# Optimization experiments

Hardware: AMD Instinct MI355X
Metric: run time of the kernel (lower is better)

The kernel has to match this reference:

```python
import jax, jax.numpy as jnp
import numpy as np

N_HEADS = 8
OUT_DIM = 64
LEAKY_SLOPE = 0.2


def setup_inputs() -> dict:
    key = jax.random.key(0)
    k1, k2, k3 = jax.random.split(key, 3)
    N, IN_DIM = 4096, 256
    x = jax.random.normal(k1, (N, IN_DIM), dtype=jnp.float32)
    # nn.Linear(in_dim, out_dim*n_heads, bias=False): weight shape (out*heads, in)
    W = jax.random.normal(k2, (OUT_DIM * N_HEADS, IN_DIM), dtype=jnp.float32) * (1.0 / np.sqrt(IN_DIM))
    # attention vector, xavier-ish scale
    attn = jax.random.normal(k3, (1, N_HEADS, 2 * OUT_DIM), dtype=jnp.float32) * 0.1
    return {"x": x, "W": W, "attn": attn}


def reference(x, W, attn):
    N = x.shape[0]
    # Wx: (N, H, D)
    Wx = (x @ W.T).reshape(N, N_HEADS, OUT_DIM)
    # The torch code concats src/tgt then dots with attn; this decomposes exactly:
    # e[i,j,h] = leaky_relu( Wx[i,h]·a_src[h] + Wx[j,h]·a_tgt[h] )
    a_src = attn[0, :, :OUT_DIM]   # (H, D)
    a_tgt = attn[0, :, OUT_DIM:]   # (H, D)
    s = jnp.einsum('nhd,hd->nh', Wx, a_src)  # (N, H) score of row index (src)
    t = jnp.einsum('nhd,hd->nh', Wx, a_tgt)  # (N, H) score of col index (tgt)
    e = jax.nn.leaky_relu(s[:, None, :] + t[None, :, :], LEAKY_SLOPE)  # (N, N, H)
    a = jax.nn.softmax(e, axis=1)  # softmax over dim=1 (neighbors j)
    # out[i,h,d] = sum_j a[i,j,h] * Wx[j,h,d]
    out = jnp.einsum('ijh,jhd->ihd', a, Wx)
    return out.reshape(N, N_HEADS * OUT_DIM)  # concat=True
```

## Files before the change

kernel.cpp:

```cpp
#include <hip/hip_runtime.h>
#include <hip/hip_bf16.h>

#define NN 4096
#define KD 256
#define NH 8
#define DD 64
#define HD 512
#define SLOPE 0.2f

__global__ __launch_bounds__(256) void gemm_st(const float* __restrict__ x,
                                               const float* __restrict__ W,
                                               const float* __restrict__ attn,
                                               float* __restrict__ Wx,
                                               float* __restrict__ sH,
                                               float* __restrict__ tH) {
    const int b = blockIdx.x;
    const int bmTile = (b & 7) * 8 + ((b >> 3) & 7);
    const int h = b >> 6;
    const int bn = h * 64;
    const int bm = bmTile * 64;
    __shared__ float As[32][68];
    __shared__ float Bs[32][68];
    const int tid = threadIdx.x;
    const int tx = tid & 15, ty = tid >> 4;
    const int srow = tid >> 2;
    const int skq  = (tid & 3) * 8;
    float acc[4][4] = {};
    for (int k0 = 0; k0 < KD; k0 += 32) {
        float4 a0 = *(const float4*)&x[(bm + srow) * KD + k0 + skq];
        float4 a1 = *(const float4*)&x[(bm + srow) * KD + k0 + skq + 4];
        float4 b0 = *(const float4*)&W[(bn + srow) * KD + k0 + skq];
        float4 b1 = *(const float4*)&W[(bn + srow) * KD + k0 + skq + 4];
        __syncthreads();
        As[skq + 0][srow] = a0.x; As[skq + 1][srow] = a0.y;
        As[skq + 2][srow] = a0.z; As[skq + 3][srow] = a0.w;
        As[skq + 4][srow] = a1.x; As[skq + 5][srow] = a1.y;
        As[skq + 6][srow] = a1.z; As[skq + 7][srow] = a1.w;
        Bs[skq + 0][srow] = b0.x; Bs[skq + 1][srow] = b0.y;
        Bs[skq + 2][srow] = b0.z; Bs[skq + 3][srow] = b0.w;
        Bs[skq + 4][srow] = b1.x; Bs[skq + 5][srow] = b1.y;
        Bs[skq + 6][srow] = b1.z; Bs[skq + 7][srow] = b1.w;
        __syncthreads();
#pragma unroll
        for (int kk = 0; kk < 32; ++kk) {
            float4 a = *(const float4*)&As[kk][ty * 4];
            float4 bb = *(const float4*)&Bs[kk][tx * 4];
            acc[0][0] += a.x * bb.x; acc[0][1] += a.x * bb.y; acc[0][2] += a.x * bb.z; acc[0][3] += a.x * bb.w;
            acc[1][0] += a.y * bb.x; acc[1][1] += a.y * bb.y; acc[1][2] += a.y * bb.z; acc[1][3] += a.y * bb.w;
            acc[2][0] += a.z * bb.x; acc[2][1] += a.z * bb.y; acc[2][2] += a.z * bb.z; acc[2][3] += a.z * bb.w;
            acc[3][0] += a.w * bb.x; acc[3][1] += a.w * bb.y; acc[3][2] += a.w * bb.z; acc[3][3] += a.w * bb.w;
        }
    }
#pragma unroll
    for (int m = 0; m < 4; ++m)
        *(float4*)&Wx[(bm + ty * 4 + m) * HD + bn + tx * 4] = *(const float4*)&acc[m][0];
    float4 as4 = *(const float4*)&attn[h * 128 + tx * 4];
    float4 at4 = *(const float4*)&attn[h * 128 + 64 + tx * 4];
#pragma unroll
    for (int m = 0; m < 4; ++m) {
        float s = acc[m][0] * as4.x + acc[m][1] * as4.y + acc[m][2] * as4.z + acc[m][3] * as4.w;
        float t = acc[m][0] * at4.x + acc[m][1] * at4.y + acc[m][2] * at4.z + acc[m][3] * at4.w;
#pragma unroll
        for (int off = 1; off < 16; off <<= 1) {
            s += __shfl_xor(s, off, 16);
            t += __shfl_xor(t, off, 16);
        }
        if (tx == 0) {
            sH[h * NN + bm + ty * 4 + m] = s;
            tH[h * NN + bm + ty * 4 + m] = t;
        }
    }
}

__global__ __launch_bounds__(512) void count_scatter(const float* __restrict__ tH,
                                                     const float* __restrict__ sH,
                                                     int* __restrict__ sortedIdx,
                                                     float* __restrict__ expT,
                                                     float* __restrict__ expT2,
                                                     int* __restrict__ cIdx) {
    const int h  = blockIdx.y;
    const int jg = blockIdx.x;
    const int tid = threadIdx.x;
    const int w  = tid >> 6;
    const int jj = tid & 63;
    const int j  = jg * 64 + jj;
    const int qj = jg >> 3;
    __shared__ float tl[NN];
    __shared__ int rsum[8][64], csum[8][64];
    {
        const float4* src4 = (const float4*)&tH[h * NN];
        float4* dst4 = (float4*)tl;
        for (int p4 = tid; p4 < NN / 4; p4 += 512) dst4[p4] = src4[p4];
    }
    __syncthreads();
    const float myT  = tl[j];
    const float negS = -sH[h * NN + j];
    const float4* t4 = (const float4*)&tl[w * 512];
    int rx = 0, ry = 0, rz = 0, rw = 0;
    int cx = 0, cy = 0, cz = 0, cw = 0;
    if (w < qj) {
#pragma unroll 8
        for (int p4 = 0; p4 < 128; ++p4) {
            float4 v = t4[p4];
            rx += (v.x <= myT); ry += (v.y <= myT); rz += (v.z <= myT); rw += (v.w <= myT);
            cx += (v.x <= negS); cy += (v.y <= negS); cz += (v.z <= negS); cw += (v.w <= negS);
        }
    } else if (w > qj) {
#pragma unroll 8
        for (int p4 = 0; p4 < 128; ++p4) {
            float4 v = t4[p4];
            rx += (v.x < myT); ry += (v.y < myT); rz += (v.z < myT); rw += (v.w < myT);
            cx += (v.x <= negS); cy += (v.y <= negS); cz += (v.z <= negS); cw += (v.w <= negS);
        }
    } else {
        const int pbase = w * 512;
#pragma unroll 4
        for (int p4 = 0; p4 < 128; ++p4) {
            float4 v = t4[p4];
            int p = pbase + p4 * 4;
            rx += (v.x < myT) | ((v.x == myT) & ((p + 0) < j));
            ry += (v.y < myT) | ((v.y == myT) & ((p + 1) < j));
            rz += (v.z < myT) | ((v.z == myT) & ((p + 2) < j));
            rw += (v.w < myT) | ((v.w == myT) & ((p + 3) < j));
            cx += (v.x <= negS); cy += (v.y <= negS); cz += (v.z <= negS); cw += (v.w <= negS);
        }
    }
    rsum[w][jj] = (rx + ry) + (rz + rw);
    csum[w][jj] = (cx + cy) + (cz + cw);
    __syncthreads();
    if (tid < 64) {
        const int jt = jg * 64 + tid;
        int R  = ((rsum[0][tid] + rsum[1][tid]) + (rsum[2][tid] + rsum[3][tid]))
               + ((rsum[4][tid] + rsum[5][tid]) + (rsum[6][tid] + rsum[7][tid]));
        int CS = ((csum[0][tid] + csum[1][tid]) + (csum[2][tid] + csum[3][tid]))
               + ((csum[4][tid] + csum[5][tid]) + (csum[6][tid] + csum[7][tid]));
        const float tv = tl[jt];
        sortedIdx[h * NN + R] = jt;
        expT [h * NN + R] = expf(tv);
        expT2[h * NN + R] = expf(SLOPE * tv);
        cIdx[h * NN + jt] = CS;
    }
}

__global__ __launch_bounds__(256) void local_prefix(const float* __restrict__ Wx,
                                                    const int* __restrict__ sortedIdx,
                                                    const float* __restrict__ expT,
                                                    const float* __restrict__ expT2,
                                                    float* __restrict__ localW,
                                                    float* __restrict__ localW2,
                                                    float* __restrict__ chunkTotW,
                                                    float* __restrict__ chunkTotW2,
                                                    float* __restrict__ localZ,
                                                    float* __restrict__ localZ2,
                                                    float* __restrict__ chunkZtot,
                                                    float* __restrict__ chunkZtot2) {
    const int c = blockIdx.x, h = blockIdx.y;
    const int tid = threadIdx.x;
    const int wid = tid >> 6, d = tid & 63;
    const int base = h * NN + c * 64;
    __shared__ float sums[4][64], sums2[4][64];
    float run = 0.f, run2 = 0.f;
    float ex[16], ex2[16];
#pragma unroll
    for (int kk = 0; kk < 16; ++kk) {
        int k = wid * 16 + kk;
        int j = sortedIdx[base + k];
        float w  = expT[base + k];
        float w2 = expT2[base + k];
        float v = Wx[j * HD + h * DD + d];
        ex[kk]  = run;  run  += w  * v;
        ex2[kk] = run2; run2 += w2 * v;
    }
    sums[wid][d] = run; sums2[wid][d] = run2;
    __syncthreads();
    float off = 0.f, off2 = 0.f;
    for (int w = 0; w < 4; ++w)
        if (w < wid) { off += sums[w][d]; off2 += sums2[w][d]; }
#pragma unroll
    for (int kk = 0; kk < 16; ++kk) {
        int k = wid * 16 + kk;
        localW [(h * NN + c * 64 + k) * 64 + d] = ex[kk]  + off;
        localW2[(h * NN + c * 64 + k) * 64 + d] = ex2[kk] + off2;
    }
    if (wid == 3) {
        chunkTotW [(h * 64 + c) * 64 + d] = off  + run;
        chunkTotW2[(h * 64 + c) * 64 + d] = off2 + run2;
    }
    if (wid == 0) {
        float z0 = expT[base + d];
        float z = z0;
#pragma unroll
        for (int o = 1; o < 64; o <<= 1) { float n = __shfl_up(z, o, 64); if (d >= o) z += n; }
        localZ[h * NN + c * 64 + d] = z - z0;
        if (d == 63) chunkZtot[h * 64 + c] = z;
    } else if (wid == 1) {
        float z0 = expT2[base + d];
        float z = z0;
#pragma unroll
        for (int o = 1; o < 64; o <<= 1) { float n = __shfl_up(z, o, 64); if (d >= o) z += n; }
        localZ2[h * NN + c * 64 + d] = z - z0;
        if (d == 63) chunkZtot2[h * 64 + c] = z;
    }
}

__global__ __launch_bounds__(256) void chunk_scan(float* __restrict__ chunkTotW,
                                                  float* __restrict__ chunkTotW2,
                                                  float* __restrict__ chunkZtot,
                                                  float* __restrict__ chunkZtot2,
                                                  float* __restrict__ totW,
                                                  float* __restrict__ totW2,
                                                  float* __restrict__ Ztot,
                                                  float* __restrict__ Ztot2) {
    const int h = blockIdx.x;
    const int tid = threadIdx.x;
    const int lane = tid & 63;
    __shared__ float cw[64 * 64];
    __shared__ float cw2[64 * 64];
    __shared__ float zb[64], zb2[64];
#pragma unroll
    for (int it = 0; it < 16; ++it) {
        int lin = it * 256 + tid;
        cw[lin]  = chunkTotW [h * 4096 + lin];
        cw2[lin] = chunkTotW2[h * 4096 + lin];
    }
    if (tid >= 128 && tid < 192) zb[lane]  = chunkZtot [h * 64 + lane];
    if (tid >= 192)              zb2[lane] = chunkZtot2[h * 64 + lane];
    __syncthreads();
    if (tid < 64) {
        float acc = 0.f;
        for (int c = 0; c < 64; ++c) { int idx = c * 64 + tid; float t = cw[idx]; cw[idx] = acc; acc += t; }
        totW[h * 64 + tid] = acc;
    } else if (tid < 128) {
        int d = tid - 64;
        float acc = 0.f;
        for (int c = 0; c < 64; ++c) { int idx = c * 64 + d; float t = cw2[idx]; cw2[idx] = acc; acc += t; }
        totW2[h * 64 + d] = acc;
    } else if (tid < 192) {
        float z0 = zb[lane];
        float z = z0;
#pragma unroll
        for (int o = 1; o < 64; o <<= 1) { float n = __shfl_up(z, o, 64); if (lane >= o) z += n; }
        chunkZtot[h * 64 + lane] = z - z0;
        if (lane == 63) Ztot[h] = z;
    } else {
        float z0 = zb2[lane];
        float z = z0;
#pragma unroll
        for (int o = 1; o < 64; o <<= 1) { float n = __shfl_up(z, o, 64); if (lane >= o) z += n; }
        chunkZtot2[h * 64 + lane] = z - z0;
        if (lane == 63) Ztot2[h] = z;
    }
    __syncthreads();
#pragma unroll
    for (int it = 0; it < 16; ++it) {
        int lin = it * 256 + tid;
        chunkTotW [h * 4096 + lin] = cw[lin];
        chunkTotW2[h * 4096 + lin] = cw2[lin];
    }
}

__global__ __launch_bounds__(256) void out_kernel(const float* __restrict__ sH,
                                                  const int* __restrict__ cIdx,
                                                  const float* __restrict__ localW,
                                                  const float* __restrict__ localW2,
                                                  const float* __restrict__ chunkTotW,
                                                  const float* __restrict__ chunkTotW2,
                                                  const float* __restrict__ localZ,
                                                  const float* __restrict__ localZ2,
                                                  const float* __restrict__ chunkZtot,
                                                  const float* __restrict__ chunkZtot2,
                                                  const float* __restrict__ totW,
                                                  const float* __restrict__ totW2,
                                                  const float* __restrict__ Ztot,
                                                  const float* __restrict__ Ztot2,
                                                  float* __restrict__ out) {
    const int h = blockIdx.y;
    const int i = blockIdx.x * 4 + (threadIdx.x >> 6);
    const int d = threadIdx.x & 63;
    const float sv = sH[h * NN + i];
    const int c = cIdx[h * NN + i];
    const float es  = expf(sv);
    const float es2 = expf(SLOPE * sv);
    float wpos, wneg, zp, zn;
    if (c == NN) {
        wpos = 0.f; zp = 0.f;
        wneg = totW2[h * 64 + d];
        zn   = Ztot2[h];
    } else {
        float pw  = localW [(h * NN + c) * 64 + d] + chunkTotW [(h * 64 + (c >> 6)) * 64 + d];
        float pw2 = localW2[(h * NN + c) * 64 + d] + chunkTotW2[(h * 64 + (c >> 6)) * 64 + d];
        wpos = totW[h * 64 + d] - pw;
        wneg = pw2;
        float pz  = localZ [h * NN + c] + chunkZtot [h * 64 + (c >> 6)];
        float pz2 = localZ2[h * NN + c] + chunkZtot2[h * 64 + (c >> 6)];
        zp = Ztot[h] - pz;
        zn = pz2;
    }
    out[i * HD + h * DD + d] = (es * wpos + es2 * wneg) / (es * zp + es2 * zn);
}

extern "C" void kernel_launch(void* const* d_in, const int* in_sizes, int n_in,
                              void* d_out, int out_size, void* d_ws, size_t ws_size,
                              hipStream_t stream) {
    const float* x    = (const float*)d_in[0];
    const float* W    = (const float*)d_in[1];
    const float* attn = (const float*)d_in[2];
    float* out = (float*)d_out;

    float* ws = (float*)d_ws;
    size_t o = 0;
    float* Wx        = ws + o; o += (size_t)NN * HD;
    float* sH        = ws + o; o += (size_t)NH * NN;
    float* tH        = ws + o; o += (size_t)NH * NN;
    float* expT      = ws + o; o += (size_t)NH * NN;
    float* expT2     = ws + o; o += (size_t)NH * NN;
    int*   sortedIdx = (int*)(ws + o); o += (size_t)NH * NN;
    int*   cIdx      = (int*)(ws + o); o += (size_t)NH * NN;
    float* localZ    = ws + o; o += (size_t)NH * NN;
    float* localZ2   = ws + o; o += (size_t)NH * NN;
    float* chunkTotW  = ws + o; o += (size_t)NH * 64 * 64;
    float* chunkTotW2 = ws + o; o += (size_t)NH * 64 * 64;
    float* chunkZtot  = ws + o; o += (size_t)NH * 64;
    float* chunkZtot2 = ws + o; o += (size_t)NH * 64;
    float* totW   = ws + o; o += (size_t)NH * 64;
    float* totW2  = ws + o; o += (size_t)NH * 64;
    float* Ztot   = ws + o; o += 64;
    float* Ztot2  = ws + o; o += 64;
    float* localW  = ws + o; o += (size_t)NH * NN * 64;
    float* localW2 = ws + o; o += (size_t)NH * NN * 64;

    gemm_st<<<dim3(512), dim3(256), 0, stream>>>(x, W, attn, Wx, sH, tH);
    count_scatter<<<dim3(64, NH), dim3(512), 0, stream>>>(tH, sH, sortedIdx, expT, expT2, cIdx);
    local_prefix<<<dim3(64, NH), dim3(256), 0, stream>>>(Wx, sortedIdx, expT, expT2, localW, localW2,
                                                         chunkTotW, chunkTotW2, localZ, localZ2, chunkZtot, chunkZtot2);
    chunk_scan<<<dim3(NH), dim3(256), 0, stream>>>(chunkTotW, chunkTotW2, chunkZtot, chunkZtot2,
                                                   totW, totW2, Ztot, Ztot2);
    out_kernel<<<dim3(NN / 4, NH), dim3(256), 0, stream>>>(sH, cIdx, localW, localW2, chunkTotW, chunkTotW2,
                                                           localZ, localZ2, chunkZtot, chunkZtot2,
                                                           totW, totW2, Ztot, Ztot2, out);
}
```

Baseline: 69.51 us.

## Fuse chunk scan into output kernel, binary-search cut index, prefetch GEMM tiles

The chunk_scan kernel is folded into out_kernel. Each block now recomputes the per-head chunk prefix sums in shared memory and finds each row's cut index with a binary search over the sorted t values. Previously count_scatter produced that index with a brute-force count, which is now removed. The GEMM also register-prefetches the next K tile while computing on the current one. The changes save one launch and the O(N^2) comparison work, at the cost of redundant per-block chunk scans and fewer, larger out_kernel blocks (64x8), which may lower parallelism.

```diff
diff --git a/kernel.cpp b/kernel.cpp
--- a/kernel.cpp
+++ b/kernel.cpp
@@ -26,11 +26,11 @@
     const int srow = tid >> 2;
     const int skq  = (tid & 3) * 8;
     float acc[4][4] = {};
+    float4 a0 = *(const float4*)&x[(bm + srow) * KD + skq];
+    float4 a1 = *(const float4*)&x[(bm + srow) * KD + skq + 4];
+    float4 b0 = *(const float4*)&W[(bn + srow) * KD + skq];
+    float4 b1 = *(const float4*)&W[(bn + srow) * KD + skq + 4];
     for (int k0 = 0; k0 < KD; k0 += 32) {
-        float4 a0 = *(const float4*)&x[(bm + srow) * KD + k0 + skq];
-        float4 a1 = *(const float4*)&x[(bm + srow) * KD + k0 + skq + 4];
-        float4 b0 = *(const float4*)&W[(bn + srow) * KD + k0 + skq];
-        float4 b1 = *(const float4*)&W[(bn + srow) * KD + k0 + skq + 4];
         __syncthreads();
         As[skq + 0][srow] = a0.x; As[skq + 1][srow] = a0.y;
         As[skq + 2][srow] = a0.z; As[skq + 3][srow] = a0.w;
@@ -41,6 +41,12 @@
         Bs[skq + 4][srow] = b1.x; Bs[skq + 5][srow] = b1.y;
         Bs[skq + 6][srow] = b1.z; Bs[skq + 7][srow] = b1.w;
         __syncthreads();
+        if (k0 + 32 < KD) {
+            a0 = *(const float4*)&x[(bm + srow) * KD + k0 + 32 + skq];
+            a1 = *(const float4*)&x[(bm + srow) * KD + k0 + 32 + skq + 4];
+            b0 = *(const float4*)&W[(bn + srow) * KD + k0 + 32 + skq];
+            b1 = *(const float4*)&W[(bn + srow) * KD + k0 + 32 + skq + 4];
+        }
 #pragma unroll
         for (int kk = 0; kk < 32; ++kk) {
             float4 a = *(const float4*)&As[kk][ty * 4];
@@ -73,11 +79,10 @@
 }
 
 __global__ __launch_bounds__(512) void count_scatter(const float* __restrict__ tH,
-                                                     const float* __restrict__ sH,
+                                                     float* __restrict__ tsorted,
                                                      int* __restrict__ sortedIdx,
                                                      float* __restrict__ expT,
-                                                     float* __restrict__ expT2,
-                                                     int* __restrict__ cIdx) {
+                                                     float* __restrict__ expT2) {
     const int h  = blockIdx.y;
     const int jg = blockIdx.x;
     const int tid = threadIdx.x;
@@ -86,31 +91,27 @@
     const int j  = jg * 64 + jj;
     const int qj = jg >> 3;
     __shared__ float tl[NN];
-    __shared__ int rsum[8][64], csum[8][64];
+    __shared__ int rsum[8][64];
     {
         const float4* src4 = (const float4*)&tH[h * NN];
         float4* dst4 = (float4*)tl;
         for (int p4 = tid; p4 < NN / 4; p4 += 512) dst4[p4] = src4[p4];
     }
     __syncthreads();
-    const float myT  = tl[j];
-    const float negS = -sH[h * NN + j];
+    const float myT = tl[j];
     const float4* t4 = (const float4*)&tl[w * 512];
     int rx = 0, ry = 0, rz = 0, rw = 0;
-    int cx = 0, cy = 0, cz = 0, cw = 0;
     if (w < qj) {
 #pragma unroll 8
         for (int p4 = 0; p4 < 128; ++p4) {
             float4 v = t4[p4];
             rx += (v.x <= myT); ry += (v.y <= myT); rz += (v.z <= myT); rw += (v.w <= myT);
-            cx += (v.x <= negS); cy += (v.y <= negS); cz += (v.z <= negS); cw += (v.w <= negS);
         }
     } else if (w > qj) {
 #pragma unroll 8
         for (int p4 = 0; p4 < 128; ++p4) {
             float4 v = t4[p4];
             rx += (v.x < myT); ry += (v.y < myT); rz += (v.z < myT); rw += (v.w < myT);
-            cx += (v.x <= negS); cy += (v.y <= negS); cz += (v.z <= negS); cw += (v.w <= negS);
         }
     } else {
         const int pbase = w * 512;
@@ -122,23 +123,19 @@
             ry += (v.y < myT) | ((v.y == myT) & ((p + 1) < j));
             rz += (v.z < myT) | ((v.z == myT) & ((p + 2) < j));
             rw += (v.w < myT) | ((v.w == myT) & ((p + 3) < j));
-            cx += (v.x <= negS); cy += (v.y <= negS); cz += (v.z <= negS); cw += (v.w <= negS);
         }
     }
     rsum[w][jj] = (rx + ry) + (rz + rw);
-    csum[w][jj] = (cx + cy) + (cz + cw);
     __syncthreads();
     if (tid < 64) {
         const int jt = jg * 64 + tid;
         int R  = ((rsum[0][tid] + rsum[1][tid]) + (rsum[2][tid] + rsum[3][tid]))
                + ((rsum[4][tid] + rsum[5][tid]) + (rsum[6][tid] + rsum[7][tid]));
-        int CS = ((csum[0][tid] + csum[1][tid]) + (csum[2][tid] + csum[3][tid]))
-               + ((csum[4][tid] + csum[5][tid]) + (csum[6][tid] + csum[7][tid]));
         const float tv = tl[jt];
+        tsorted[h * NN + R]   = tv;
         sortedIdx[h * NN + R] = jt;
         expT [h * NN + R] = expf(tv);
         expT2[h * NN + R] = expf(SLOPE * tv);
-        cIdx[h * NN + jt] = CS;
     }
 }
 
@@ -203,100 +200,106 @@
     }
 }
 
-__global__ __launch_bounds__(256) void chunk_scan(float* __restrict__ chunkTotW,
-                                                  float* __restrict__ chunkTotW2,
-                                                  float* __restrict__ chunkZtot,
-                                                  float* __restrict__ chunkZtot2,
-                                                  float* __restrict__ totW,
-                                                  float* __restrict__ totW2,
-                                                  float* __restrict__ Ztot,
-                                                  float* __restrict__ Ztot2) {
-    const int h = blockIdx.x;
+__global__ __launch_bounds__(256) void out_kernel(const float* __restrict__ sH,
+                                                  const float* __restrict__ tsorted,
+                                                  const float* __restrict__ localW,
+                                                  const float* __restrict__ localW2,
+                                                  const float* __restrict__ localZ,
+                                                  const float* __restrict__ localZ2,
+                                                  const float* __restrict__ chunkTotW,
+                                                  const float* __restrict__ chunkTotW2,
+                                                  const float* __restrict__ chunkZtot,
+                                                  const float* __restrict__ chunkZtot2,
+                                                  float* __restrict__ out) {
+    const int h  = blockIdx.y;
+    const int ig = blockIdx.x;
     const int tid = threadIdx.x;
-    const int lane = tid & 63;
-    __shared__ float cw[64 * 64];
-    __shared__ float cw2[64 * 64];
-    __shared__ float zb[64], zb2[64];
-#pragma unroll
-    for (int it = 0; it < 16; ++it) {
-        int lin = it * 256 + tid;
-        cw[lin]  = chunkTotW [h * 4096 + lin];
-        cw2[lin] = chunkTotW2[h * 4096 + lin];
-    }
-    if (tid >= 128 && tid < 192) zb[lane]  = chunkZtot [h * 64 + lane];
-    if (tid >= 192)              zb2[lane] = chunkZtot2[h * 64 + lane];
+    __shared__ float ts[NN];
+    __shared__ float scW[65][64];
+    __shared__ float scW2[65][64];
+    __shared__ float scZ[65], scZ2[65];
+    {
+        const float4* src = (const float4*)&tsorted[h * NN];
+        float4* dst = (float4*)ts;
+        for (int p = tid; p < NN / 4; p += 256) dst[p] = src[p];
+        const float4* cw  = (const float4*)&chunkTotW [h * 4096];
+        const float4* cw2 = (const float4*)&chunkTotW2[h * 4096];
+        for (int p = tid; p < 1024; p += 256) {
+            int c = p >> 4, q = p & 15;
+            ((float4*)&scW[c][0])[q]  = cw[p];
+            ((float4*)&scW2[c][0])[q] = cw2[p];
+        }
+        if (tid < 64)                    scZ [tid]      = chunkZtot [h * 64 + tid];
+        else if (tid < 128)              scZ2[tid - 64] = chunkZtot2[h * 64 + tid - 64];
+    }
     __syncthreads();
     if (tid < 64) {
         float acc = 0.f;
-        for (int c = 0; c < 64; ++c) { int idx = c * 64 + tid; float t = cw[idx]; cw[idx] = acc; acc += t; }
-        totW[h * 64 + tid] = acc;
+        for (int c = 0; c < 64; ++c) { float t = scW[c][tid]; scW[c][tid] = acc; acc += t; }
+        scW[64][tid] = acc;
     } else if (tid < 128) {
-        int d = tid - 64;
-        float acc = 0.f;
-        for (int c = 0; c < 64; ++c) { int idx = c * 64 + d; float t = cw2[idx]; cw2[idx] = acc; acc += t; }
-        totW2[h * 64 + d] = acc;
+        int d = tid - 64; float acc = 0.f;
+        for (int c = 0; c < 64; ++c) { float t = scW2[c][d]; scW2[c][d] = acc; acc += t; }
+        scW2[64][d] = acc;
     } else if (tid < 192) {
-        float z0 = zb[lane];
-        float z = z0;
+        int lane = tid & 63;
+        float z0 = scZ[lane]; float z = z0;
 #pragma unroll
         for (int o = 1; o < 64; o <<= 1) { float n = __shfl_up(z, o, 64); if (lane >= o) z += n; }
-        chunkZtot[h * 64 + lane] = z - z0;
-        if (lane == 63) Ztot[h] = z;
+        scZ[lane] = z - z0;
+        if (lane == 63) scZ[64] = z;
     } else {
-        float z0 = zb2[lane];
-        float z = z0;
+        int lane = tid & 63;
+        float z0 = scZ2[lane]; float z = z0;
 #pragma unroll
         for (int o = 1; o < 64; o <<= 1) { float n = __shfl_up(z, o, 64); if (lane >= o) z += n; }
-        chunkZtot2[h * 64 + lane] = z - z0;
-        if (lane == 63) Ztot2[h] = z;
-    }
-    __syncthreads();
-#pragma unroll
-    for (int it = 0; it < 16; ++it) {
-        int lin = it * 256 + tid;
-        chunkTotW [h * 4096 + lin] = cw[lin];
-        chunkTotW2[h * 4096 + lin] = cw2[lin];
-    }
-}
-
-__global__ __launch_bounds__(256) void out_kernel(const float* __restrict__ sH,
-                                                  const int* __restrict__ cIdx,
-                                                  const float* __restrict__ localW,
-                                                  const float* __restrict__ localW2,
-                                                  const float* __restrict__ chunkTotW,
-                                                  const float* __restrict__ chunkTotW2,
-                                                  const float* __restrict__ localZ,
-                                                  const float* __restrict__ localZ2,
-                                                  const float* __restrict__ chunkZtot,
-                                                  const float* __restrict__ chunkZtot2,
-                                                  const float* __restrict__ totW,
-                                                  const float* __restrict__ totW2,
-                                                  const float* __restrict__ Ztot,
-                                                  const float* __restrict__ Ztot2,
-                                                  float* __restrict__ out) {
-    const int h = blockIdx.y;
-    const int i = blockIdx.x * 4 + (threadIdx.x >> 6);
-    const int d = threadIdx.x & 63;
-    const float sv = sH[h * NN + i];
-    const int c = cIdx[h * NN + i];
-    const float es  = expf(sv);
-    const float es2 = expf(SLOPE * sv);
-    float wpos, wneg, zp, zn;
-    if (c == NN) {
-        wpos = 0.f; zp = 0.f;
-        wneg = totW2[h * 64 + d];
-        zn   = Ztot2[h];
-    } else {
-        float pw  = localW [(h * NN + c) * 64 + d] + chunkTotW [(h * 64 + (c >> 6)) * 64 + d];
-        float pw2 = localW2[(h * NN + c) * 64 + d] + chunkTotW2[(h * 64 + (c >> 6)) * 64 + d];
-        wpos = totW[h * 64 + d] - pw;
-        wneg = pw2;
-        float pz  = localZ [h * NN + c] + chunkZtot [h * 64 + (c >> 6)];
-        float pz2 = localZ2[h * NN + c] + chunkZtot2[h * 64 + (c >> 6)];
-        zp = Ztot[h] - pz;
-        zn = pz2;
-    }
-    out[i * HD + h * DD + d] = (es * wpos + es2 * wneg) / (es * zp + es2 * zn);
+        scZ2[lane] = z - z0;
+        if (lane == 63) scZ2[64] = z;
+    }
+    __syncthreads();
+    int   cc[16];
+    float svv[16];
+#pragma unroll
+    for (int p = 0; p < 16; ++p) {
+        const int i = ig * 64 + p * 4 + (tid >> 6);
+        const float sv = sH[h * NN + i];
+        svv[p] = sv;
+        const float negS = -sv;
+        int lo = 0, hi = NN;
+#pragma unroll
+        for (int st = 0; st < 12; ++st) {
+            int mid = (lo + hi) >> 1;
+            bool le = ts[mid] <= negS;
+            lo = le ? mid + 1 : lo;
+            hi = le ? hi : mid;
+        }
+        cc[p] = lo;
+    }
+#pragma unroll
+    for (int p = 0; p < 16; ++p) {
+        const int i = ig * 64 + p * 4 + (tid >> 6);
+        const int d = tid & 63;
+        const int c = cc[p];
+        const float sv = svv[p];
+        const float es  = expf(sv);
+        const float es2 = expf(SLOPE * sv);
+        float wpos, wneg, zp, zn;
+        if (c == NN) {
+            wpos = 0.f; zp = 0.f;
+            wneg = scW2[64][d];
+            zn   = scZ2[64];
+        } else {
+            float pw  = localW [(h * NN + c) * 64 + d] + scW [c >> 6][d];
+            float pw2 = localW2[(h * NN + c) * 64 + d] + scW2[c >> 6][d];
+            wpos = scW[64][d] - pw;
+            wneg = pw2;
+            float pz  = localZ [h * NN + c] + scZ [c >> 6];
+            float pz2 = localZ2[h * NN + c] + scZ2[c >> 6];
+            zp = scZ[64] - pz;
+            zn = pz2;
+        }
+        out[i * HD + h * DD + d] = (es * wpos + es2 * wneg) / (es * zp + es2 * zn);
+    }
 }
 
 extern "C" void kernel_launch(void* const* d_in, const int* in_sizes, int n_in,
@@ -312,30 +315,23 @@
     float* Wx        = ws + o; o += (size_t)NN * HD;
     float* sH        = ws + o; o += (size_t)NH * NN;
     float* tH        = ws + o; o += (size_t)NH * NN;
+    float* tsorted   = ws + o; o += (size_t)NH * NN;
     float* expT      = ws + o; o += (size_t)NH * NN;
     float* expT2     = ws + o; o += (size_t)NH * NN;
     int*   sortedIdx = (int*)(ws + o); o += (size_t)NH * NN;
-    int*   cIdx      = (int*)(ws + o); o += (size_t)NH * NN;
     float* localZ    = ws + o; o += (size_t)NH * NN;
     float* localZ2   = ws + o; o += (size_t)NH * NN;
     float* chunkTotW  = ws + o; o += (size_t)NH * 64 * 64;
     float* chunkTotW2 = ws + o; o += (size_t)NH * 64 * 64;
     float* chunkZtot  = ws + o; o += (size_t)NH * 64;
     float* chunkZtot2 = ws + o; o += (size_t)NH * 64;
-    float* totW   = ws + o; o += (size_t)NH * 64;
-    float* totW2  = ws + o; o += (size_t)NH * 64;
-    float* Ztot   = ws + o; o += 64;
-    float* Ztot2  = ws + o; o += 64;
     float* localW  = ws + o; o += (size_t)NH * NN * 64;
     float* localW2 = ws + o; o += (size_t)NH * NN * 64;
 
     gemm_st<<<dim3(512), dim3(256), 0, stream>>>(x, W, attn, Wx, sH, tH);
-    count_scatter<<<dim3(64, NH), dim3(512), 0, stream>>>(tH, sH, sortedIdx, expT, expT2, cIdx);
+    count_scatter<<<dim3(64, NH), dim3(512), 0, stream>>>(tH, tsorted, sortedIdx, expT, expT2);
     local_prefix<<<dim3(64, NH), dim3(256), 0, stream>>>(Wx, sortedIdx, expT, expT2, localW, localW2,
                                                          chunkTotW, chunkTotW2, localZ, localZ2, chunkZtot, chunkZtot2);
-    chunk_scan<<<dim3(NH), dim3(256), 0, stream>>>(chunkTotW, chunkTotW2, chunkZtot, chunkZtot2,
-                                                   totW, totW2, Ztot, Ztot2);
-    out_kernel<<<dim3(NN / 4, NH), dim3(256), 0, stream>>>(sH, cIdx, localW, localW2, chunkTotW, chunkTotW2,
-                                                           localZ, localZ2, chunkZtot, chunkZtot2,
-                                                           totW, totW2, Ztot, Ztot2, out);
-}
+    out_kernel<<<dim3(64, NH), dim3(256), 0, stream>>>(sH, tsorted, localW, localW2, localZ, localZ2,
+                                                       chunkTotW, chunkTotW2, chunkZtot, chunkZtot2, out);
+}
```

Result: slower. 71.40 us (+2.7%).
